# Performance work log

Hardware: AMD Instinct MI355X
Metric: run time of the kernel (lower is better)

Reference implementation:

```python
import jax, jax.numpy as jnp
import numpy as np

B, S, D = 4, 2048, 1024
H, DH = 16, 64
THETA = 10000.0


def _rope_tables(seq_len, dim):
    # freqs_cis = exp(i * t * f), here as cos/sin tables, shape [S, dim//2]
    freqs = 1.0 / (THETA ** (jnp.arange(0, dim, 2, dtype=jnp.float32) / dim))
    ang = jnp.outer(jnp.arange(seq_len, dtype=jnp.float32), freqs)
    return jnp.cos(ang), jnp.sin(ang)


def _apply_rope(x, cos, sin):
    # x: [B,S,H,DH]; pairs are interleaved (x[...,2i], x[...,2i+1])
    xe = x[..., 0::2]
    xo = x[..., 1::2]
    c = cos[None, :, None, :]
    s = sin[None, :, None, :]
    out = jnp.stack([xe * c - xo * s, xe * s + xo * c], axis=-1)
    return out.reshape(x.shape).astype(x.dtype)


def setup_inputs() -> dict:
    key = jax.random.key(0)
    ks = jax.random.split(key, 5)
    x = jax.random.normal(ks[0], (B, S, D), dtype=jnp.float32)
    Wq = jax.random.normal(ks[1], (D, D), dtype=jnp.float32) * 0.02
    Wk = jax.random.normal(ks[2], (D, D), dtype=jnp.float32) * 0.02
    Wv = jax.random.normal(ks[3], (D, D), dtype=jnp.float32) * 0.02
    Wo = jax.random.normal(ks[4], (D, D), dtype=jnp.float32) * 0.02
    lambdas = jnp.zeros((2,), dtype=jnp.float32)
    return {"x": x, "Wq": Wq, "Wk": Wk, "Wv": Wv, "Wo": Wo, "lambdas": lambdas}


def reference(x, Wq, Wk, Wv, Wo, lambdas):
    scale = 1.0 / np.sqrt(DH)
    q = (x @ Wq.T).reshape(B, S, H, DH)
    k = (x @ Wk.T).reshape(B, S, H, DH)
    v = (x @ Wv.T).reshape(B, S, H, DH)
    cos, sin = _rope_tables(S, DH)
    q = _apply_rope(q, cos, sin)
    k = _apply_rope(k, cos, sin)
    # explicit QK^T with causal mask, softmax, then @V (dropout is identity in eval)
    attn = jnp.einsum('bshd,bthd->bhst', q, k) * scale  # [B,H,S,S]
    causal = jnp.tril(jnp.ones((S, S), dtype=bool))
    attn = jnp.where(causal[None, None], attn, -jnp.inf)
    probs = jax.nn.softmax(attn, axis=-1)
    head_out = jnp.einsum('bhst,bthd->bshd', probs, v)  # [B,S,H,DH]
    out = head_out.reshape(B, S, D) @ Wo.T
    return out
```

## Files before the change

### kernel.cpp

```cpp
#include <hip/hip_runtime.h>
#include <math.h>

static constexpr int Bsz = 4, Sq = 2048, Dm = 1024, NH = 16, DHd = 64;
static constexpr int Mrows = Bsz * Sq;
static constexpr float ROPE_LN = 0.14391156831212787f;

typedef _Float16 half8 __attribute__((ext_vector_type(8)));
typedef _Float16 half4v __attribute__((ext_vector_type(4)));
typedef float f32x4 __attribute__((ext_vector_type(4)));

__device__ __forceinline__ void gl_lds16(const void* g, void* l) {
    __builtin_amdgcn_global_load_lds(
        (const __attribute__((address_space(1))) void*)g,
        (__attribute__((address_space(3))) void*)l, 16, 0, 0);
}

__global__ __launch_bounds__(256) void prep_kernel(
    const float* __restrict__ x,
    const float* __restrict__ Wq, const float* __restrict__ Wk,
    const float* __restrict__ Wv, const float* __restrict__ Wo,
    _Float16* __restrict__ xh,
    _Float16* __restrict__ Wqh, _Float16* __restrict__ Wkh,
    _Float16* __restrict__ Wvh, _Float16* __restrict__ Woh,
    float2* __restrict__ rope)
{
    const int i = blockIdx.x * 256 + threadIdx.x;
    if (i < 2097152) {
        const float4 v = ((const float4*)x)[i];
        half4v hv;
        hv[0] = (_Float16)v.x; hv[1] = (_Float16)v.y;
        hv[2] = (_Float16)v.z; hv[3] = (_Float16)v.w;
        ((half4v*)xh)[i] = hv;
    } else if (i < 3145728) {
        const int w = (i - 2097152) >> 18;
        const int off = (i - 2097152) & 262143;
        const float* s = (w == 0) ? Wq : (w == 1) ? Wk : (w == 2) ? Wv : Wo;
        _Float16* d = (w == 0) ? Wqh : (w == 1) ? Wkh : (w == 2) ? Wvh : Woh;
        const float sc = (w == 0) ? 0.125f : 1.0f;
        const float4 v = ((const float4*)s)[off];
        half4v hv;
        hv[0] = (_Float16)(v.x * sc); hv[1] = (_Float16)(v.y * sc);
        hv[2] = (_Float16)(v.z * sc); hv[3] = (_Float16)(v.w * sc);
        ((half4v*)d)[off] = hv;
    } else {
        const int t = i - 3145728;
        const int pos = t >> 5, j = t & 31;
        const float f = expf(-ROPE_LN * (float)(2 * j));
        const float a = (float)pos * f;
        rope[t] = make_float2(cosf(a), sinf(a));
    }
}

template <typename OutT, int MODE>
__device__ __forceinline__ void mfma_gemm_body(
    const _Float16* __restrict__ A, const _Float16* __restrict__ W,
    OutT* __restrict__ C, const float2* __restrict__ rope, int K, int N)
{
    __shared__ _Float16 As[2][128 * 32];
    __shared__ _Float16 Bs[2][128 * 32];

    const int tid = threadIdx.x;
    const int wave = tid >> 6, lane = tid & 63;
    const int quad = lane >> 4, l16 = lane & 15;
    const int wm = (wave >> 1) * 64, wn = (wave & 1) * 64;
    const int m0 = blockIdx.y * 128, n0 = blockIdx.x * 128;

    const _Float16* gA[2]; const _Float16* gB[2];
    int lOff[2];
    #pragma unroll
    for (int i = 0; i < 2; ++i) {
        const int F = (wave * 2 + i) * 64 + lane;
        const int r = F >> 2, cp = F & 3;
        const int c = cp ^ ((r >> 1) & 3);
        gA[i] = A + (size_t)(m0 + r) * K + c * 8;
        gB[i] = W + (size_t)(n0 + r) * K + c * 8;
        lOff[i] = (wave * 2 + i) * 512;
    }

    const int sw = (l16 >> 1) & 3;
    int offA[4], offB[4];
    #pragma unroll
    for (int t = 0; t < 4; ++t) {
        offA[t] = (wm + t * 16 + l16) * 32 + ((quad ^ sw) * 8);
        offB[t] = (wn + t * 16 + l16) * 32 + ((quad ^ sw) * 8);
    }

    f32x4 acc[4][4];
    #pragma unroll
    for (int im = 0; im < 4; ++im)
        #pragma unroll
        for (int nb = 0; nb < 4; ++nb)
            #pragma unroll
            for (int r = 0; r < 4; ++r) acc[im][nb][r] = 0.f;

    auto stage = [&](int buf, int koff) {
        #pragma unroll
        for (int i = 0; i < 2; ++i) {
            gl_lds16(gA[i] + koff, &As[buf][lOff[i]]);
            gl_lds16(gB[i] + koff, &Bs[buf][lOff[i]]);
        }
    };
    auto compute = [&](int buf) {
        half8 a[4], b[4];
        #pragma unroll
        for (int t = 0; t < 4; ++t) {
            a[t] = *(const half8*)&As[buf][offA[t]];
            b[t] = *(const half8*)&Bs[buf][offB[t]];
        }
        #pragma unroll
        for (int im = 0; im < 4; ++im)
            #pragma unroll
            for (int nb = 0; nb < 4; ++nb)
                acc[im][nb] = __builtin_amdgcn_mfma_f32_16x16x32_f16(
                    a[im], b[nb], acc[im][nb], 0, 0, 0);
    };

    stage(0, 0);

    for (int k0 = 0; k0 < K; k0 += 64) {
        __syncthreads();
        stage(1, k0 + 32);
        compute(0);
        __syncthreads();
        if (k0 + 64 < K) stage(0, k0 + 64);
        compute(1);
    }

    #pragma unroll
    for (int nb = 0; nb < 4; ++nb) {
        const int n = n0 + wn + nb * 16 + l16;
        if constexpr (MODE == 2) {
            const int hb = ((m0 + wm) >> 11) * 16 + (n >> 6);
            const int dh = n & 63;
            const int tb = (m0 + wm) & (Sq - 1);
            half8 v0, v1;
            #pragma unroll
            for (int r = 0; r < 4; ++r)
                #pragma unroll
                for (int im = 0; im < 4; ++im) {
                    const int idx = r * 4 + im;
                    const _Float16 h = (_Float16)acc[im][nb][r];
                    if (idx < 8) v0[idx] = h; else v1[idx - 8] = h;
                }
            _Float16* dst = C + (((size_t)hb * 64 + dh) << 11) + tb + quad * 16;
            *(half8*)dst = v0;
            *(half8*)(dst + 8) = v1;
        } else {
            const int j = (n & 63) >> 1;
            #pragma unroll
            for (int im = 0; im < 4; ++im) {
                #pragma unroll
                for (int r = 0; r < 4; ++r) {
                    const int m = m0 + wm + im * 16 + quad * 4 + r;
                    float v = acc[im][nb][r];
                    if constexpr (MODE == 1) {
                        const int pos = m & (Sq - 1);
                        const float2 cs = rope[pos * 32 + j];
                        const float vp = __shfl_xor(v, 1);
                        v = (n & 1) ? (vp * cs.y + v * cs.x)
                                    : (v * cs.x - vp * cs.y);
                        C[(size_t)m * N + n] = (_Float16)v;
                    } else {
                        C[(size_t)m * N + n] = v;
                    }
                }
            }
        }
    }
}

__global__ __launch_bounds__(256) void qkv_mfma_kernel(
    const _Float16* __restrict__ xh,
    const _Float16* __restrict__ Wq, const _Float16* __restrict__ Wk,
    const _Float16* __restrict__ Wv,
    _Float16* __restrict__ Qo, _Float16* __restrict__ Ko,
    _Float16* __restrict__ VTp, const float2* __restrict__ rope)
{
    const int z = blockIdx.z;
    if (z == 0)
        mfma_gemm_body<_Float16, 1>(xh, Wq, Qo, rope, Dm, Dm);
    else if (z == 1)
        mfma_gemm_body<_Float16, 1>(xh, Wk, Ko, rope, Dm, Dm);
    else
        mfma_gemm_body<_Float16, 2>(xh, Wv, VTp, nullptr, Dm, Dm);
}

__global__ __launch_bounds__(256) void oproj_mfma_kernel(
    const _Float16* __restrict__ HOh, const _Float16* __restrict__ Wo,
    float* __restrict__ out)
{
    mfma_gemm_body<float, 0>(HOh, Wo, out, nullptr, Dm, Dm);
}

__global__ __launch_bounds__(256) void attn_mfma_kernel(
    const _Float16* __restrict__ Q, const _Float16* __restrict__ K,
    const _Float16* __restrict__ VT, _Float16* __restrict__ HO)
{
    __shared__ _Float16 Ks[2][64 * 64];
    __shared__ _Float16 Vs[2][64 * 64];
    __shared__ _Float16 Ps[4][16][72];

    const int tid = threadIdx.x;
    const int wave = tid >> 6, lane = tid & 63;
    const int quad = lane >> 4, l16 = lane & 15;
    const int id = blockIdx.x;
    const int hb = id & 63;
    const int qi = 31 - (id >> 6);
    const int h = hb & 15, b = hb >> 4;
    const int q0 = qi * 64;
    const size_t base = (size_t)b * Sq * Dm + (size_t)h * DHd;
    const size_t vtbase = (size_t)hb * 64 * Sq;

    half8 ones;
    #pragma unroll
    for (int i = 0; i < 8; ++i) ones[i] = (_Float16)1.0f;

    half8 aQ[2];
    {
        const _Float16* qrow =
            Q + base + (size_t)(q0 + wave * 16 + l16) * Dm + quad * 8;
        aQ[0] = *(const half8*)(qrow);
        aQ[1] = *(const half8*)(qrow + 32);
    }

    f32x4 Oacc[4];
    #pragma unroll
    for (int nb = 0; nb < 4; ++nb)
        #pragma unroll
        for (int r = 0; r < 4; ++r) Oacc[nb][r] = 0.f;
    f32x4 lacc;
    #pragma unroll
    for (int r = 0; r < 4; ++r) lacc[r] = 0.f;

    auto stage_tile = [&](int t0, int buf) {
        #pragma unroll
        for (int i = 0; i < 2; ++i) {
            const int F = (wave * 2 + i) * 64 + lane;
            const int r = F >> 3;
            const int cl = (F & 7) ^ (r & 7);
            gl_lds16(K + base + (size_t)(t0 + r) * Dm + cl * 8,
                     &Ks[buf][(wave * 2 + i) * 512]);
            gl_lds16(VT + vtbase + ((size_t)r << 11) + t0 + cl * 8,
                     &Vs[buf][(wave * 2 + i) * 512]);
        }
    };

    auto do_tile = [&](int buf, bool diag) {
        const _Float16* Kb = Ks[buf];
        const _Float16* Vb = Vs[buf];

        f32x4 sacc[4];
        #pragma unroll
        for (int nb = 0; nb < 4; ++nb)
            #pragma unroll
            for (int r = 0; r < 4; ++r) sacc[nb][r] = 0.f;
        #pragma unroll
        for (int kstep = 0; kstep < 2; ++kstep) {
            #pragma unroll
            for (int nb = 0; nb < 4; ++nb) {
                const int krow = nb * 16 + l16;
                const int kch = (kstep * 4 + quad) ^ (krow & 7);
                const half8 bK = *(const half8*)&Kb[krow * 64 + kch * 8];
                sacc[nb] = __builtin_amdgcn_mfma_f32_16x16x32_f16(
                    aQ[kstep], bK, sacc[nb], 0, 0, 0);
            }
        }

        #pragma unroll
        for (int r = 0; r < 4; ++r) {
            half4v pk;
            #pragma unroll
            for (int nb = 0; nb < 4; ++nb) {
                float v = sacc[nb][r];
                if (diag && (nb * 16 + l16 > wave * 16 + quad * 4 + r))
                    v = -1.0e4f;
                pk[nb] = (_Float16)__expf(v);
            }
            *(half4v*)&Ps[wave][quad * 4 + r][l16 * 4] = pk;
        }

        #pragma unroll
        for (int kstep = 0; kstep < 2; ++kstep) {
            const half8 aP =
                *(const half8*)&Ps[wave][l16][kstep * 32 + quad * 8];
            lacc = __builtin_amdgcn_mfma_f32_16x16x32_f16(
                aP, ones, lacc, 0, 0, 0);
            #pragma unroll
            for (int nb = 0; nb < 4; ++nb) {
                const int vrow = nb * 16 + l16;
                const int vch = (kstep * 4 + quad) ^ (vrow & 7);
                const half8 bV = *(const half8*)&Vb[vrow * 64 + vch * 8];
                Oacc[nb] = __builtin_amdgcn_mfma_f32_16x16x32_f16(
                    aP, bV, Oacc[nb], 0, 0, 0);
            }
        }
    };

    stage_tile(0, 0);
    for (int t = 0; t <= qi; ++t) {
        __syncthreads();
        if (t < qi) stage_tile((t + 1) * 64, (t + 1) & 1);
        do_tile(t & 1, t == qi);
    }

    float inv[4];
    #pragma unroll
    for (int r = 0; r < 4; ++r) inv[r] = 1.0f / lacc[r];
    #pragma unroll
    for (int nb = 0; nb < 4; ++nb)
        #pragma unroll
        for (int r = 0; r < 4; ++r) {
            const int row = wave * 16 + quad * 4 + r;
            HO[base + (size_t)(q0 + row) * Dm + nb * 16 + l16] =
                (_Float16)(Oacc[nb][r] * inv[r]);
        }
}

extern "C" void kernel_launch(void* const* d_in, const int* in_sizes, int n_in,
                              void* d_out, int out_size, void* d_ws, size_t ws_size,
                              hipStream_t stream)
{
    const float* x  = (const float*)d_in[0];
    const float* Wq = (const float*)d_in[1];
    const float* Wk = (const float*)d_in[2];
    const float* Wv = (const float*)d_in[3];
    const float* Wo = (const float*)d_in[4];
    float* out = (float*)d_out;

    const size_t matX = (size_t)Mrows * Dm;
    const size_t matW = (size_t)Dm * Dm;

    _Float16* xh  = (_Float16*)d_ws;
    _Float16* Wqh = xh + matX;
    _Float16* Wkh = Wqh + matW;
    _Float16* Wvh = Wkh + matW;
    _Float16* Woh = Wvh + matW;
    _Float16* Qh  = Woh + matW;
    _Float16* Kh  = Qh + matX;
    _Float16* VTp = Kh + matX;
    _Float16* HOh = VTp + matX;
    float2* rope  = (float2*)(HOh + matX);

    dim3 blk(256);
    prep_kernel<<<(3145728 + 65536) / 256, blk, 0, stream>>>(
        x, Wq, Wk, Wv, Wo, xh, Wqh, Wkh, Wvh, Woh, rope);
    qkv_mfma_kernel<<<dim3(Dm / 128, Mrows / 128, 3), blk, 0, stream>>>(
        xh, Wqh, Wkh, Wvh, Qh, Kh, VTp, rope);
    attn_mfma_kernel<<<dim3(32 * NH * Bsz), blk, 0, stream>>>(
        Qh, Kh, VTp, HOh);
    oproj_mfma_kernel<<<dim3(Dm / 128, Mrows / 128, 1), blk, 0, stream>>>(
        HOh, Woh, out);
}
```

Measured before the change: 271.2 us.

## Widen attention Q tile to 128 rows and single-buffer GEMM LDS

```diff
diff --git a/kernel.cpp b/kernel.cpp
--- a/kernel.cpp
+++ b/kernel.cpp
@@ -56,8 +56,8 @@
     const _Float16* __restrict__ A, const _Float16* __restrict__ W,
     OutT* __restrict__ C, const float2* __restrict__ rope, int K, int N)
 {
-    __shared__ _Float16 As[2][128 * 32];
-    __shared__ _Float16 Bs[2][128 * 32];
+    __shared__ _Float16 As[128 * 32];
+    __shared__ _Float16 Bs[128 * 32];
 
     const int tid = threadIdx.x;
     const int wave = tid >> 6, lane = tid & 63;
@@ -66,7 +66,7 @@
     const int m0 = blockIdx.y * 128, n0 = blockIdx.x * 128;
 
     const _Float16* gA[2]; const _Float16* gB[2];
-    int lOff[2];
+    _Float16* lA[2]; _Float16* lB[2];
     #pragma unroll
     for (int i = 0; i < 2; ++i) {
         const int F = (wave * 2 + i) * 64 + lane;
@@ -74,7 +74,8 @@
         const int c = cp ^ ((r >> 1) & 3);
         gA[i] = A + (size_t)(m0 + r) * K + c * 8;
         gB[i] = W + (size_t)(n0 + r) * K + c * 8;
-        lOff[i] = (wave * 2 + i) * 512;
+        lA[i] = As + (wave * 2 + i) * 512;
+        lB[i] = Bs + (wave * 2 + i) * 512;
     }
 
     const int sw = (l16 >> 1) & 3;
@@ -93,19 +94,20 @@
             #pragma unroll
             for (int r = 0; r < 4; ++r) acc[im][nb][r] = 0.f;
 
-    auto stage = [&](int buf, int koff) {
+    for (int k0 = 0; k0 < K; k0 += 32) {
+        __syncthreads();
         #pragma unroll
         for (int i = 0; i < 2; ++i) {
-            gl_lds16(gA[i] + koff, &As[buf][lOff[i]]);
-            gl_lds16(gB[i] + koff, &Bs[buf][lOff[i]]);
-        }
-    };
-    auto compute = [&](int buf) {
+            gl_lds16(gA[i] + k0, lA[i]);
+            gl_lds16(gB[i] + k0, lB[i]);
+        }
+        __syncthreads();
+
         half8 a[4], b[4];
         #pragma unroll
         for (int t = 0; t < 4; ++t) {
-            a[t] = *(const half8*)&As[buf][offA[t]];
-            b[t] = *(const half8*)&Bs[buf][offB[t]];
+            a[t] = *(const half8*)&As[offA[t]];
+            b[t] = *(const half8*)&Bs[offB[t]];
         }
         #pragma unroll
         for (int im = 0; im < 4; ++im)
@@ -113,17 +115,6 @@
             for (int nb = 0; nb < 4; ++nb)
                 acc[im][nb] = __builtin_amdgcn_mfma_f32_16x16x32_f16(
                     a[im], b[nb], acc[im][nb], 0, 0, 0);
-    };
-
-    stage(0, 0);
-
-    for (int k0 = 0; k0 < K; k0 += 64) {
-        __syncthreads();
-        stage(1, k0 + 32);
-        compute(0);
-        __syncthreads();
-        if (k0 + 64 < K) stage(0, k0 + 64);
-        compute(1);
     }
 
     #pragma unroll
@@ -198,16 +189,16 @@
 {
     __shared__ _Float16 Ks[2][64 * 64];
     __shared__ _Float16 Vs[2][64 * 64];
-    __shared__ _Float16 Ps[4][16][72];
+    __shared__ _Float16 Ps[4][32][72];
 
     const int tid = threadIdx.x;
     const int wave = tid >> 6, lane = tid & 63;
     const int quad = lane >> 4, l16 = lane & 15;
     const int id = blockIdx.x;
     const int hb = id & 63;
-    const int qi = 31 - (id >> 6);
+    const int qi = 15 - (id >> 6);
     const int h = hb & 15, b = hb >> 4;
-    const int q0 = qi * 64;
+    const int q0 = qi * 128;
     const size_t base = (size_t)b * Sq * Dm + (size_t)h * DHd;
     const size_t vtbase = (size_t)hb * 64 * Sq;
 
@@ -215,22 +206,27 @@
     #pragma unroll
     for (int i = 0; i < 8; ++i) ones[i] = (_Float16)1.0f;
 
-    half8 aQ[2];
-    {
+    half8 aQ[2][2];
+    #pragma unroll
+    for (int mf = 0; mf < 2; ++mf) {
         const _Float16* qrow =
-            Q + base + (size_t)(q0 + wave * 16 + l16) * Dm + quad * 8;
-        aQ[0] = *(const half8*)(qrow);
-        aQ[1] = *(const half8*)(qrow + 32);
-    }
-
-    f32x4 Oacc[4];
-    #pragma unroll
-    for (int nb = 0; nb < 4; ++nb)
-        #pragma unroll
-        for (int r = 0; r < 4; ++r) Oacc[nb][r] = 0.f;
-    f32x4 lacc;
-    #pragma unroll
-    for (int r = 0; r < 4; ++r) lacc[r] = 0.f;
+            Q + base + (size_t)(q0 + wave * 32 + mf * 16 + l16) * Dm + quad * 8;
+        aQ[mf][0] = *(const half8*)(qrow);
+        aQ[mf][1] = *(const half8*)(qrow + 32);
+    }
+
+    f32x4 Oacc[2][4];
+    #pragma unroll
+    for (int mf = 0; mf < 2; ++mf)
+        #pragma unroll
+        for (int nb = 0; nb < 4; ++nb)
+            #pragma unroll
+            for (int r = 0; r < 4; ++r) Oacc[mf][nb][r] = 0.f;
+    f32x4 lacc[2];
+    #pragma unroll
+    for (int mf = 0; mf < 2; ++mf)
+        #pragma unroll
+        for (int r = 0; r < 4; ++r) lacc[mf][r] = 0.f;
 
     auto stage_tile = [&](int t0, int buf) {
         #pragma unroll
@@ -245,15 +241,18 @@
         }
     };
 
-    auto do_tile = [&](int buf, bool diag) {
+    auto do_tile = [&](int buf, int dd, bool diag) {
         const _Float16* Kb = Ks[buf];
         const _Float16* Vb = Vs[buf];
 
-        f32x4 sacc[4];
-        #pragma unroll
-        for (int nb = 0; nb < 4; ++nb)
-            #pragma unroll
-            for (int r = 0; r < 4; ++r) sacc[nb][r] = 0.f;
+        f32x4 sacc[2][4];
+        #pragma unroll
+        for (int mf = 0; mf < 2; ++mf)
+            #pragma unroll
+            for (int nb = 0; nb < 4; ++nb)
+                #pragma unroll
+                for (int r = 0; r < 4; ++r) sacc[mf][nb][r] = 0.f;
+        __builtin_amdgcn_s_setprio(1);
         #pragma unroll
         for (int kstep = 0; kstep < 2; ++kstep) {
             #pragma unroll
@@ -261,59 +260,77 @@
                 const int krow = nb * 16 + l16;
                 const int kch = (kstep * 4 + quad) ^ (krow & 7);
                 const half8 bK = *(const half8*)&Kb[krow * 64 + kch * 8];
-                sacc[nb] = __builtin_amdgcn_mfma_f32_16x16x32_f16(
-                    aQ[kstep], bK, sacc[nb], 0, 0, 0);
-            }
-        }
-
-        #pragma unroll
-        for (int r = 0; r < 4; ++r) {
-            half4v pk;
-            #pragma unroll
-            for (int nb = 0; nb < 4; ++nb) {
-                float v = sacc[nb][r];
-                if (diag && (nb * 16 + l16 > wave * 16 + quad * 4 + r))
-                    v = -1.0e4f;
-                pk[nb] = (_Float16)__expf(v);
-            }
-            *(half4v*)&Ps[wave][quad * 4 + r][l16 * 4] = pk;
-        }
-
+                #pragma unroll
+                for (int mf = 0; mf < 2; ++mf)
+                    sacc[mf][nb] = __builtin_amdgcn_mfma_f32_16x16x32_f16(
+                        aQ[mf][kstep], bK, sacc[mf][nb], 0, 0, 0);
+            }
+        }
+        __builtin_amdgcn_s_setprio(0);
+
+        #pragma unroll
+        for (int mf = 0; mf < 2; ++mf)
+            #pragma unroll
+            for (int r = 0; r < 4; ++r) {
+                half4v pk;
+                #pragma unroll
+                for (int nb = 0; nb < 4; ++nb) {
+                    float v = sacc[mf][nb][r];
+                    if (diag && (nb * 16 + l16 + dd >
+                                 wave * 32 + mf * 16 + quad * 4 + r))
+                        v = -1.0e4f;
+                    pk[nb] = (_Float16)__expf(v);
+                }
+                *(half4v*)&Ps[wave][mf * 16 + quad * 4 + r][l16 * 4] = pk;
+            }
+
+        __builtin_amdgcn_s_setprio(1);
         #pragma unroll
         for (int kstep = 0; kstep < 2; ++kstep) {
-            const half8 aP =
-                *(const half8*)&Ps[wave][l16][kstep * 32 + quad * 8];
-            lacc = __builtin_amdgcn_mfma_f32_16x16x32_f16(
-                aP, ones, lacc, 0, 0, 0);
+            half8 aP[2];
+            #pragma unroll
+            for (int mf = 0; mf < 2; ++mf) {
+                aP[mf] = *(const half8*)
+                    &Ps[wave][mf * 16 + l16][kstep * 32 + quad * 8];
+                lacc[mf] = __builtin_amdgcn_mfma_f32_16x16x32_f16(
+                    aP[mf], ones, lacc[mf], 0, 0, 0);
+            }
             #pragma unroll
             for (int nb = 0; nb < 4; ++nb) {
                 const int vrow = nb * 16 + l16;
                 const int vch = (kstep * 4 + quad) ^ (vrow & 7);
                 const half8 bV = *(const half8*)&Vb[vrow * 64 + vch * 8];
-                Oacc[nb] = __builtin_amdgcn_mfma_f32_16x16x32_f16(
-                    aP, bV, Oacc[nb], 0, 0, 0);
-            }
-        }
+                #pragma unroll
+                for (int mf = 0; mf < 2; ++mf)
+                    Oacc[mf][nb] = __builtin_amdgcn_mfma_f32_16x16x32_f16(
+                        aP[mf], bV, Oacc[mf][nb], 0, 0, 0);
+            }
+        }
+        __builtin_amdgcn_s_setprio(0);
     };
 
+    const int nt = 2 * qi + 2;
     stage_tile(0, 0);
-    for (int t = 0; t <= qi; ++t) {
+    for (int t = 0; t < nt; ++t) {
         __syncthreads();
-        if (t < qi) stage_tile((t + 1) * 64, (t + 1) & 1);
-        do_tile(t & 1, t == qi);
-    }
-
-    float inv[4];
-    #pragma unroll
-    for (int r = 0; r < 4; ++r) inv[r] = 1.0f / lacc[r];
-    #pragma unroll
-    for (int nb = 0; nb < 4; ++nb)
-        #pragma unroll
-        for (int r = 0; r < 4; ++r) {
-            const int row = wave * 16 + quad * 4 + r;
-            HO[base + (size_t)(q0 + row) * Dm + nb * 16 + l16] =
-                (_Float16)(Oacc[nb][r] * inv[r]);
-        }
+        if (t + 1 < nt) stage_tile((t + 1) * 64, (t + 1) & 1);
+        do_tile(t & 1, t * 64 - q0, t >= nt - 2);
+    }
+
+    #pragma unroll
+    for (int mf = 0; mf < 2; ++mf) {
+        float inv[4];
+        #pragma unroll
+        for (int r = 0; r < 4; ++r) inv[r] = 1.0f / lacc[mf][r];
+        #pragma unroll
+        for (int nb = 0; nb < 4; ++nb)
+            #pragma unroll
+            for (int r = 0; r < 4; ++r) {
+                const int row = wave * 32 + mf * 16 + quad * 4 + r;
+                HO[base + (size_t)(q0 + row) * Dm + nb * 16 + l16] =
+                    (_Float16)(Oacc[mf][nb][r] * inv[r]);
+            }
+    }
 }
 
 extern "C" void kernel_launch(void* const* d_in, const int* in_sizes, int n_in,
@@ -346,7 +363,7 @@
         x, Wq, Wk, Wv, Wo, xh, Wqh, Wkh, Wvh, Woh, rope);
     qkv_mfma_kernel<<<dim3(Dm / 128, Mrows / 128, 3), blk, 0, stream>>>(
         xh, Wqh, Wkh, Wvh, Qh, Kh, VTp, rope);
-    attn_mfma_kernel<<<dim3(32 * NH * Bsz), blk, 0, stream>>>(
+    attn_mfma_kernel<<<dim3(16 * NH * Bsz), blk, 0, stream>>>(
         Qh, Kh, VTp, HOh);
     oproj_mfma_kernel<<<dim3(Dm / 128, Mrows / 128, 1), blk, 0, stream>>>(
         HOh, Woh, out);
```

Result: faster. 264.4 us (-2.5%).
